# Optimization experiments

Measured on AMD Instinct MI355X. Metric: run time of the kernel, lower is better.

## Reference

```python
import jax, jax.numpy as jnp
import numpy as np

B, T, C = 4, 2048, 1024
NH = 16
HD = C // NH  # 64


def setup_inputs() -> dict:
    key = jax.random.key(0)
    k1, k2, k3 = jax.random.split(key, 3)
    x = jax.random.normal(k1, (B, T, C), dtype=jnp.float32)
    # causal mask buffer, 1 = keep, 0 = mask out
    mask = jnp.tril(jnp.ones((T, T), dtype=jnp.int32))[None, None, :, :]
    # learned params (Linear with bias=False): torch stores weight as [out, in],
    # y = x @ W.T ; we store transposed for direct matmul
    w_qkv = jax.random.normal(k2, (C, 3 * C), dtype=jnp.float32) / np.sqrt(C)
    w_proj = jax.random.normal(k3, (C, C), dtype=jnp.float32) / np.sqrt(C)
    return {"x": x, "mask": mask, "w_qkv": w_qkv, "w_proj": w_proj}


def reference(x, mask, w_qkv, w_proj):
    b, t, c = x.shape
    qkv = x @ w_qkv  # [b, t, 3c]
    q, k, v = jnp.split(qkv, 3, axis=-1)
    # [b, nh, t, hd]
    q = q.reshape(b, t, NH, HD).transpose(0, 2, 1, 3)
    k = k.reshape(b, t, NH, HD).transpose(0, 2, 1, 3)
    v = v.reshape(b, t, NH, HD).transpose(0, 2, 1, 3)
    att = jnp.einsum("bhqd,bhkd->bhqk", q, k) * (1.0 / np.sqrt(HD))
    att = jnp.where(mask == 0, -jnp.inf, att)
    att = jax.nn.softmax(att, axis=-1)
    y = jnp.einsum("bhqk,bhkd->bhqd", att, v)
    y = y.transpose(0, 2, 1, 3).reshape(b, t, c)
    return y @ w_proj
```

## Files before the change

kernel.cpp:

```cpp
#include <hip/hip_runtime.h>
#include <hip/hip_bf16.h>

typedef _Float16 f16;
typedef __attribute__((ext_vector_type(4))) _Float16 f16x4;
typedef __attribute__((ext_vector_type(8))) _Float16 f16x8;
typedef __attribute__((ext_vector_type(4))) float f32x4;

#define MFMA16(a, b, c) __builtin_amdgcn_mfma_f32_16x16x16f16((a), (b), (c), 0, 0, 0)
#define MFMA32(a, b, c) __builtin_amdgcn_mfma_f32_16x16x32_f16((a), (b), (c), 0, 0, 0)
#define EXP2(x) __builtin_amdgcn_exp2f(x)
#define GLOAD_LDS16(g, l)                                                        \
  __builtin_amdgcn_global_load_lds((const __attribute__((address_space(1))) void*)(g), \
                                   (__attribute__((address_space(3))) void*)(l), 16, 0, 0)
typedef const __attribute__((address_space(3))) char* lds_cp;
#define TR16(dst, addr, imm) \
  asm volatile("ds_read_b64_tr_b16 %0, %1 offset:" imm : "=v"(dst) : "v"(addr))

__device__ __forceinline__ float max3f(float a, float b, float c) {
  return fmaxf(fmaxf(a, b), c);
}

__global__ __launch_bounds__(256) void prep_kernel(
    const float* __restrict__ x, f16* __restrict__ x16,
    const float* __restrict__ wq, f16* __restrict__ wqT,
    const float* __restrict__ wp, f16* __restrict__ wpT) {
  const int blk = blockIdx.x;
  const int tid = threadIdx.x;
  if (blk < 8192) {
    int i = blk * 256 + tid;
    const float4 v = reinterpret_cast<const float4*>(x)[i];
    f16x4 h;
    h[0] = (f16)v.x; h[1] = (f16)v.y; h[2] = (f16)v.z; h[3] = (f16)v.w;
    reinterpret_cast<f16x4*>(x16)[i] = h;
    return;
  }
  const float* src;
  f16* dst;
  int R, Cc, bx, by;
  if (blk < 11264) {
    int j = blk - 8192;
    bx = j % 96; by = j / 96;
    src = wq; dst = wqT; R = 1024; Cc = 3072;
  } else {
    int j = blk - 11264;
    bx = j & 31; by = j >> 5;
    src = wp; dst = wpT; R = 1024; Cc = 1024;
  }
  __shared__ float t[32][33];
  int tx0 = bx * 32, ty0 = by * 32;
  int c = tid & 31;
  int r0 = tid >> 5;
#pragma unroll
  for (int i = 0; i < 4; i++) {
    int r = r0 + 8 * i;
    t[r][c] = src[(size_t)(ty0 + r) * Cc + tx0 + c];
  }
  __syncthreads();
#pragma unroll
  for (int i = 0; i < 4; i++) {
    int a = r0 + 8 * i;
    dst[(size_t)(tx0 + a) * R + ty0 + c] = (f16)t[c][a];
  }
}

template <bool OUT_F32>
__global__ __launch_bounds__(512, 2) void gemm_deep_kernel(
    const f16* __restrict__ A, const f16* __restrict__ Bt, void* __restrict__ Cout,
    int M, int N, int K) {
  __shared__ __align__(16) char smem[147456];
  const int tid = threadIdx.x;
  const int lane = tid & 63, wid = tid >> 6;
  const int wm = wid >> 2, wn = wid & 3;
  const int lo = lane & 15, hi = lane >> 4;

  const int ntn = N >> 7;
  const int nwg = (M >> 8) * ntn;
  const int wg = (blockIdx.x & 7) * (nwg >> 3) + (blockIdx.x >> 3);
  const int tm0 = (wg / ntn) << 8;
  const int tn0 = (wg % ntn) << 7;

  const int prow = tid >> 3;
  const int u8 = (tid & 7) ^ (prow & 7);
  const f16* asrc[4];
  const f16* bsrc[2];
#pragma unroll
  for (int c = 0; c < 4; c++) asrc[c] = A + (size_t)(tm0 + c * 64 + prow) * K + u8 * 8;
#pragma unroll
  for (int c = 0; c < 2; c++) bsrc[c] = Bt + (size_t)(tn0 + c * 64 + prow) * K + u8 * 8;

  const int swz = lo & 7;
  const int s0 = (hi ^ swz) << 4, s1 = ((4 + hi) ^ swz) << 4;
  const int abase0 = wm * 16384 + lo * 128 + s0;
  const int abase1 = wm * 16384 + lo * 128 + s1;
  int boff0[2], boff1[2];
#pragma unroll
  for (int ni = 0; ni < 2; ni++) {
    int g = 2 * wn + ni;
    int base = 32768 + (g >> 2) * 8192 + ((g & 3) * 16 + lo) * 128;
    boff0[ni] = base + s0;
    boff1[ni] = base + s1;
  }

  f32x4 acc[8][2] = {};

  auto stage = [&](int kt, char* buf) {
    const int ke = kt << 6;
#pragma unroll
    for (int c = 0; c < 4; c++)
      GLOAD_LDS16(asrc[c] + ke, buf + c * 8192 + tid * 16);
#pragma unroll
    for (int c = 0; c < 2; c++)
      GLOAD_LDS16(bsrc[c] + ke, buf + 32768 + c * 8192 + tid * 16);
  };

  const int NT = K >> 6;
  stage(0, smem);
  stage(1, smem + 49152);

  int bufi = 0;
  for (int t = 0; t < NT; t++) {
    char* db = smem + bufi * 49152;
    if (t + 1 < NT) {
      asm volatile("s_waitcnt vmcnt(6)" ::: "memory");
    } else {
      asm volatile("s_waitcnt vmcnt(0)" ::: "memory");
    }
    __builtin_amdgcn_s_barrier();
    if (t + 2 < NT) {
      int nb = bufi + 2;
      if (nb >= 3) nb -= 3;
      stage(t + 2, smem + nb * 49152);
    }
    __builtin_amdgcn_sched_barrier(0);

    f16x8 a[8][2], b[2][2];
#pragma unroll
    for (int mi = 0; mi < 8; mi++) {
      int off = (mi >> 2) * 8192 + (mi & 3) * 2048;
      a[mi][0] = *(const f16x8*)(db + abase0 + off);
      a[mi][1] = *(const f16x8*)(db + abase1 + off);
    }
#pragma unroll
    for (int ni = 0; ni < 2; ni++) {
      b[ni][0] = *(const f16x8*)(db + boff0[ni]);
      b[ni][1] = *(const f16x8*)(db + boff1[ni]);
    }
    __builtin_amdgcn_s_setprio(1);
#pragma unroll
    for (int mi = 0; mi < 8; mi++)
#pragma unroll
      for (int ni = 0; ni < 2; ni++) {
        acc[mi][ni] = MFMA32(a[mi][0], b[ni][0], acc[mi][ni]);
        acc[mi][ni] = MFMA32(a[mi][1], b[ni][1], acc[mi][ni]);
      }
    __builtin_amdgcn_s_setprio(0);

    bufi = (bufi == 2) ? 0 : bufi + 1;
  }

#pragma unroll
  for (int mi = 0; mi < 8; mi++)
#pragma unroll
    for (int ni = 0; ni < 2; ni++)
#pragma unroll
      for (int r = 0; r < 4; r++) {
        int row = tm0 + wm * 128 + mi * 16 + 4 * hi + r;
        int col = tn0 + wn * 32 + ni * 16 + lo;
        float v = acc[mi][ni][r];
        if (OUT_F32)
          ((float*)Cout)[(size_t)row * N + col] = v;
        else
          ((f16*)Cout)[(size_t)row * N + col] = (f16)v;
      }
}

__global__ __launch_bounds__(256, 4) void attn_kernel(
    const f16* __restrict__ qkv, f16* __restrict__ y) {
  constexpr int T = 2048, NHD = 3072, LDO = 72;
  const int bh = blockIdx.x;
  const int b = bh >> 4, h = bh & 15;
  const int pr = blockIdx.y;
  const int tid = threadIdx.x;
  const int lane = tid & 63, w = tid >> 6;
  const int lo = lane & 15, hi = lane >> 4;

  const size_t base = (size_t)b * T * NHD + (size_t)h * 64;
  const f16* Qp = qkv + base;
  const f16* Kp = qkv + base + 1024;
  const f16* Vp = qkv + base + 2048;

  __shared__ __align__(16) char smem[32768];
  f16 (*Ol)[LDO] = (f16(*)[LDO])smem;

  const int tile[2] = {pr, 31 - pr};
  const int qb[2] = {tile[0] * 64 + w * 16, tile[1] * 64 + w * 16};

  const float scf = 0.125f * 1.44269504089f;
  f16x8 qf[2][2];
#pragma unroll
  for (int s = 0; s < 2; s++) {
    const f16* qrow = Qp + (size_t)(qb[s] + lo) * NHD;
#pragma unroll
    for (int ks = 0; ks < 2; ks++) {
      f16x8 v = *(const f16x8*)&qrow[ks * 32 + 8 * hi];
#pragma unroll
      for (int j = 0; j < 8; j++) v[j] = (f16)((float)v[j] * scf);
      qf[s][ks] = v;
    }
  }

  f32x4 oacc[2][4] = {};
  f32x4 lacc[2] = {};
  float mreg[2] = {-1e30f, -1e30f};
  const f16x4 ones4 = {(f16)1.f, (f16)1.f, (f16)1.f, (f16)1.f};

  const int kr = tid >> 3;
  const int kslot = (tid & 7) ^ (kr & 7);
  const int tp = tid & 127;
  const int vkey = 4 * (tp >> 3) + ((tp >> 1) & 3);
  const int vcol = (tid >> 7) * 16 + (tid & 1) * 8;

  const int kfo0 = lo * 64 + ((hi ^ (lo & 7)) * 8);
  const int kfo1 = lo * 64 + (((4 + hi) ^ (lo & 7)) * 8);

  auto stage = [&](int kv, int c) {
    char* kb = smem + c * 8192;
    char* vb = smem + 16384 + c * 8192;
    GLOAD_LDS16(&Kp[(size_t)(kv + kr) * NHD + kslot * 8], kb + tid * 16);
    GLOAD_LDS16(&Kp[(size_t)(kv + kr + 32) * NHD + kslot * 8], kb + 4096 + tid * 16);
    GLOAD_LDS16(&Vp[(size_t)(kv + vkey) * NHD + vcol], vb + tid * 16);
    GLOAD_LDS16(&Vp[(size_t)(kv + vkey) * NHD + vcol + 32], vb + 4096 + tid * 16);
  };

  const int nt = 32 - pr;
  stage(0, 0);
  asm volatile("s_waitcnt vmcnt(0)" ::: "memory");
  __builtin_amdgcn_s_barrier();

  for (int t = 0; t < nt; t++) {
    const int cur = t & 1;
    const int kv0 = t * 64;
    if (t + 1 < nt) stage(kv0 + 64, cur ^ 1);

    const f16* Kl = (const f16*)(smem + cur * 8192);
    const bool act0 = kv0 <= qb[0] + 15;

    f16x8 kf[2][4];
#pragma unroll
    for (int ct = 0; ct < 4; ct++) {
      kf[0][ct] = *(const f16x8*)&Kl[ct * 1024 + kfo0];
      kf[1][ct] = *(const f16x8*)&Kl[ct * 1024 + kfo1];
    }

    f16x4 pb[2][4];
#pragma unroll
    for (int s = 0; s < 2; s++) {
      if (s == 0 && !act0) continue;
      f32x4 s_[4] = {};
      __builtin_amdgcn_s_setprio(1);
#pragma unroll
      for (int ks = 0; ks < 2; ks++)
#pragma unroll
        for (int ct = 0; ct < 4; ct++)
          s_[ct] = MFMA32(kf[ks][ct], qf[s][ks], s_[ct]);
      __builtin_amdgcn_s_setprio(0);

      if (kv0 + 63 > qb[s]) {
        const int q = qb[s] + lo;
#pragma unroll
        for (int ct = 0; ct < 4; ct++)
#pragma unroll
          for (int r = 0; r < 4; r++)
            if (kv0 + ct * 16 + 4 * hi + r > q) s_[ct][r] = -3.0e38f;
      }
      float t0 = max3f(s_[0][0], s_[0][1], s_[0][2]);
      float t1 = max3f(s_[0][3], s_[1][0], s_[1][1]);
      float t2 = max3f(s_[1][2], s_[1][3], s_[2][0]);
      float t3 = max3f(s_[2][1], s_[2][2], s_[2][3]);
      float t4 = max3f(s_[3][0], s_[3][1], s_[3][2]);
      float mt = fmaxf(max3f(t0, t1, t2), max3f(t3, t4, s_[3][3]));
      mt = fmaxf(mt, __shfl_xor(mt, 16));
      mt = fmaxf(mt, __shfl_xor(mt, 32));
      float mn = mreg[s];
      if (!__all(mt <= mn + 8.f)) {
        mn = fmaxf(mn, mt);
        const float al = EXP2(mreg[s] - mn);
        mreg[s] = mn;
#pragma unroll
        for (int r = 0; r < 4; r++) lacc[s][r] *= al;
#pragma unroll
        for (int ct = 0; ct < 4; ct++)
#pragma unroll
          for (int r = 0; r < 4; r++) oacc[s][ct][r] *= al;
      }
#pragma unroll
      for (int ct = 0; ct < 4; ct++)
#pragma unroll
        for (int r = 0; r < 4; r++)
          pb[s][ct][r] = (f16)EXP2(s_[ct][r] - mn);
      __builtin_amdgcn_s_setprio(1);
#pragma unroll
      for (int kk = 0; kk < 4; kk++)
        lacc[s] = MFMA16(ones4, pb[s][kk], lacc[s]);
      __builtin_amdgcn_s_setprio(0);
    }

    lds_cp vtrb = (lds_cp)(smem + 16384 + cur * 8192) + lane * 8;
#pragma unroll
    for (int ct = 0; ct < 4; ct++) {
      lds_cp bct = vtrb + ct * 2048;
      f16x4 v0, v1, v2, v3;
      TR16(v0, bct, "0");
      TR16(v1, bct, "512");
      TR16(v2, bct, "1024");
      TR16(v3, bct, "1536");
      asm volatile("s_waitcnt lgkmcnt(0)" ::: "memory");
      __builtin_amdgcn_sched_barrier(0);
      __builtin_amdgcn_s_setprio(1);
      if (act0) {
        oacc[0][ct] = MFMA16(v0, pb[0][0], oacc[0][ct]);
        oacc[0][ct] = MFMA16(v1, pb[0][1], oacc[0][ct]);
        oacc[0][ct] = MFMA16(v2, pb[0][2], oacc[0][ct]);
        oacc[0][ct] = MFMA16(v3, pb[0][3], oacc[0][ct]);
      }
      oacc[1][ct] = MFMA16(v0, pb[1][0], oacc[1][ct]);
      oacc[1][ct] = MFMA16(v1, pb[1][1], oacc[1][ct]);
      oacc[1][ct] = MFMA16(v2, pb[1][2], oacc[1][ct]);
      oacc[1][ct] = MFMA16(v3, pb[1][3], oacc[1][ct]);
      __builtin_amdgcn_s_setprio(0);
    }

    asm volatile("s_waitcnt vmcnt(0)" ::: "memory");
    __builtin_amdgcn_s_barrier();
  }

#pragma unroll
  for (int s = 0; s < 2; s++) {
    __syncthreads();
    const float inv = 1.f / lacc[s][0];
#pragma unroll
    for (int ct = 0; ct < 4; ct++) {
      f16x4 o4;
#pragma unroll
      for (int r = 0; r < 4; r++) o4[r] = (f16)(oacc[s][ct][r] * inv);
      *(f16x4*)&Ol[w * 16 + lo][ct * 16 + 4 * hi] = o4;
    }
    __syncthreads();
#pragma unroll
    for (int i = 0; i < 2; i++) {
      int idx = tid + 256 * i;
      int qq = idx >> 3, ch = idx & 7;
      *(f16x8*)&y[((size_t)b * T + tile[s] * 64 + qq) * 1024 + (size_t)h * 64 + ch * 8] =
          *(const f16x8*)&Ol[qq][ch * 8];
    }
  }
}

extern "C" void kernel_launch(void* const* d_in, const int* in_sizes, int n_in,
                              void* d_out, int out_size, void* d_ws, size_t ws_size,
                              hipStream_t stream) {
  const float* x = (const float*)d_in[0];
  const float* w_qkv = (const float*)d_in[2];
  const float* w_proj = (const float*)d_in[3];

  constexpr int B = 4, T = 2048, C = 1024, NH = 16;
  constexpr int M = B * T;
  constexpr int N1 = 3 * C;

  char* ws = (char*)d_ws;
  f16* x16 = (f16*)ws;    ws += (size_t)M * C * 2;
  f16* wqkvT = (f16*)ws;  ws += (size_t)N1 * C * 2;
  f16* wprojT = (f16*)ws; ws += (size_t)C * C * 2;
  f16* qkvb = (f16*)ws;   ws += (size_t)M * N1 * 2;
  f16* y16 = (f16*)ws;

  prep_kernel<<<12288, 256, 0, stream>>>(x, x16, w_qkv, wqkvT, w_proj, wprojT);
  gemm_deep_kernel<false><<<(M / 256) * (N1 / 128), 512, 0, stream>>>(x16, wqkvT, qkvb, M, N1, C);
  attn_kernel<<<dim3(B * NH, 16), 256, 0, stream>>>(qkvb, y16);
  gemm_deep_kernel<true><<<(M / 256) * (C / 128), 512, 0, stream>>>(y16, wprojT, (float*)d_out, M, C, C);
}
```

Measured before the change: 172.6 us.

## Reorder attention inner loop to issue both QK MFMAs first and interleave softmax with PV

Restructures the per-tile loop so both sub-tiles' QK^T MFMAs are issued back to back. Each sub-tile's softmax is then immediately followed by its own PV accumulation instead of doing all softmax before all PV. The fp32-to-f16 conversion of probabilities now uses packed round-toward-zero conversion. The aim is to overlap MFMA latency with exp/max ALU work and cut conversion instructions, at the cost of holding more score registers live and slightly different rounding. V fragments are now read from LDS twice per tile, once per sub-tile.

```diff
diff --git a/kernel.cpp b/kernel.cpp
--- a/kernel.cpp
+++ b/kernel.cpp
@@ -2,6 +2,7 @@
 #include <hip/hip_bf16.h>
 
 typedef _Float16 f16;
+typedef __attribute__((ext_vector_type(2))) __fp16 fp16x2;
 typedef __attribute__((ext_vector_type(4))) _Float16 f16x4;
 typedef __attribute__((ext_vector_type(8))) _Float16 f16x8;
 typedef __attribute__((ext_vector_type(4))) float f32x4;
@@ -232,80 +233,52 @@
     GLOAD_LDS16(&Vp[(size_t)(kv + vkey) * NHD + vcol + 32], vb + 4096 + tid * 16);
   };
 
-  const int nt = 32 - pr;
-  stage(0, 0);
-  asm volatile("s_waitcnt vmcnt(0)" ::: "memory");
-  __builtin_amdgcn_s_barrier();
-
-  for (int t = 0; t < nt; t++) {
-    const int cur = t & 1;
-    const int kv0 = t * 64;
-    if (t + 1 < nt) stage(kv0 + 64, cur ^ 1);
-
-    const f16* Kl = (const f16*)(smem + cur * 8192);
-    const bool act0 = kv0 <= qb[0] + 15;
-
-    f16x8 kf[2][4];
+  auto softmax_fin = [&](f32x4* sv, int si, f16x4* pbv, int kv0) {
+    if (kv0 + 63 > qb[si]) {
+      const int q = qb[si] + lo;
+#pragma unroll
+      for (int ct = 0; ct < 4; ct++)
+#pragma unroll
+        for (int r = 0; r < 4; r++)
+          if (kv0 + ct * 16 + 4 * hi + r > q) sv[ct][r] = -3.0e38f;
+    }
+    float t0 = max3f(sv[0][0], sv[0][1], sv[0][2]);
+    float t1 = max3f(sv[0][3], sv[1][0], sv[1][1]);
+    float t2 = max3f(sv[1][2], sv[1][3], sv[2][0]);
+    float t3 = max3f(sv[2][1], sv[2][2], sv[2][3]);
+    float t4 = max3f(sv[3][0], sv[3][1], sv[3][2]);
+    float mt = fmaxf(max3f(t0, t1, t2), max3f(t3, t4, sv[3][3]));
+    mt = fmaxf(mt, __shfl_xor(mt, 16));
+    mt = fmaxf(mt, __shfl_xor(mt, 32));
+    float mn = mreg[si];
+    if (!__all(mt <= mn + 8.f)) {
+      mn = fmaxf(mn, mt);
+      const float al = EXP2(mreg[si] - mn);
+      mreg[si] = mn;
+#pragma unroll
+      for (int r = 0; r < 4; r++) lacc[si][r] *= al;
+#pragma unroll
+      for (int ct = 0; ct < 4; ct++)
+#pragma unroll
+        for (int r = 0; r < 4; r++) oacc[si][ct][r] *= al;
+    }
 #pragma unroll
     for (int ct = 0; ct < 4; ct++) {
-      kf[0][ct] = *(const f16x8*)&Kl[ct * 1024 + kfo0];
-      kf[1][ct] = *(const f16x8*)&Kl[ct * 1024 + kfo1];
-    }
-
-    f16x4 pb[2][4];
-#pragma unroll
-    for (int s = 0; s < 2; s++) {
-      if (s == 0 && !act0) continue;
-      f32x4 s_[4] = {};
-      __builtin_amdgcn_s_setprio(1);
-#pragma unroll
-      for (int ks = 0; ks < 2; ks++)
-#pragma unroll
-        for (int ct = 0; ct < 4; ct++)
-          s_[ct] = MFMA32(kf[ks][ct], qf[s][ks], s_[ct]);
-      __builtin_amdgcn_s_setprio(0);
-
-      if (kv0 + 63 > qb[s]) {
-        const int q = qb[s] + lo;
-#pragma unroll
-        for (int ct = 0; ct < 4; ct++)
-#pragma unroll
-          for (int r = 0; r < 4; r++)
-            if (kv0 + ct * 16 + 4 * hi + r > q) s_[ct][r] = -3.0e38f;
-      }
-      float t0 = max3f(s_[0][0], s_[0][1], s_[0][2]);
-      float t1 = max3f(s_[0][3], s_[1][0], s_[1][1]);
-      float t2 = max3f(s_[1][2], s_[1][3], s_[2][0]);
-      float t3 = max3f(s_[2][1], s_[2][2], s_[2][3]);
-      float t4 = max3f(s_[3][0], s_[3][1], s_[3][2]);
-      float mt = fmaxf(max3f(t0, t1, t2), max3f(t3, t4, s_[3][3]));
-      mt = fmaxf(mt, __shfl_xor(mt, 16));
-      mt = fmaxf(mt, __shfl_xor(mt, 32));
-      float mn = mreg[s];
-      if (!__all(mt <= mn + 8.f)) {
-        mn = fmaxf(mn, mt);
-        const float al = EXP2(mreg[s] - mn);
-        mreg[s] = mn;
-#pragma unroll
-        for (int r = 0; r < 4; r++) lacc[s][r] *= al;
-#pragma unroll
-        for (int ct = 0; ct < 4; ct++)
-#pragma unroll
-          for (int r = 0; r < 4; r++) oacc[s][ct][r] *= al;
-      }
-#pragma unroll
-      for (int ct = 0; ct < 4; ct++)
-#pragma unroll
-        for (int r = 0; r < 4; r++)
-          pb[s][ct][r] = (f16)EXP2(s_[ct][r] - mn);
-      __builtin_amdgcn_s_setprio(1);
-#pragma unroll
-      for (int kk = 0; kk < 4; kk++)
-        lacc[s] = MFMA16(ones4, pb[s][kk], lacc[s]);
-      __builtin_amdgcn_s_setprio(0);
-    }
-
-    lds_cp vtrb = (lds_cp)(smem + 16384 + cur * 8192) + lane * 8;
+      float p0 = EXP2(sv[ct][0] - mn), p1 = EXP2(sv[ct][1] - mn);
+      float p2 = EXP2(sv[ct][2] - mn), p3 = EXP2(sv[ct][3] - mn);
+      union { f16x4 v; fp16x2 h[2]; } u;
+      u.h[0] = __builtin_amdgcn_cvt_pkrtz(p0, p1);
+      u.h[1] = __builtin_amdgcn_cvt_pkrtz(p2, p3);
+      pbv[ct] = u.v;
+    }
+    __builtin_amdgcn_s_setprio(1);
+#pragma unroll
+    for (int kk = 0; kk < 4; kk++)
+      lacc[si] = MFMA16(ones4, pbv[kk], lacc[si]);
+    __builtin_amdgcn_s_setprio(0);
+  };
+
+  auto pv_sub = [&](int si, f16x4* pbv, lds_cp vtrb) {
 #pragma unroll
     for (int ct = 0; ct < 4; ct++) {
       lds_cp bct = vtrb + ct * 2048;
@@ -317,17 +290,67 @@
       asm volatile("s_waitcnt lgkmcnt(0)" ::: "memory");
       __builtin_amdgcn_sched_barrier(0);
       __builtin_amdgcn_s_setprio(1);
-      if (act0) {
-        oacc[0][ct] = MFMA16(v0, pb[0][0], oacc[0][ct]);
-        oacc[0][ct] = MFMA16(v1, pb[0][1], oacc[0][ct]);
-        oacc[0][ct] = MFMA16(v2, pb[0][2], oacc[0][ct]);
-        oacc[0][ct] = MFMA16(v3, pb[0][3], oacc[0][ct]);
-      }
-      oacc[1][ct] = MFMA16(v0, pb[1][0], oacc[1][ct]);
-      oacc[1][ct] = MFMA16(v1, pb[1][1], oacc[1][ct]);
-      oacc[1][ct] = MFMA16(v2, pb[1][2], oacc[1][ct]);
-      oacc[1][ct] = MFMA16(v3, pb[1][3], oacc[1][ct]);
+      oacc[si][ct] = MFMA16(v0, pbv[0], oacc[si][ct]);
+      oacc[si][ct] = MFMA16(v1, pbv[1], oacc[si][ct]);
+      oacc[si][ct] = MFMA16(v2, pbv[2], oacc[si][ct]);
+      oacc[si][ct] = MFMA16(v3, pbv[3], oacc[si][ct]);
       __builtin_amdgcn_s_setprio(0);
+    }
+  };
+
+  const int nt = 32 - pr;
+  stage(0, 0);
+  asm volatile("s_waitcnt vmcnt(0)" ::: "memory");
+  __builtin_amdgcn_s_barrier();
+
+  for (int t = 0; t < nt; t++) {
+    const int cur = t & 1;
+    const int kv0 = t * 64;
+    if (t + 1 < nt) stage(kv0 + 64, cur ^ 1);
+
+    const f16* Kl = (const f16*)(smem + cur * 8192);
+    const bool act0 = kv0 <= qb[0] + 15;
+
+    f16x8 kf[2][4];
+#pragma unroll
+    for (int ct = 0; ct < 4; ct++) {
+      kf[0][ct] = *(const f16x8*)&Kl[ct * 1024 + kfo0];
+      kf[1][ct] = *(const f16x8*)&Kl[ct * 1024 + kfo1];
+    }
+
+    lds_cp vtrb = (lds_cp)(smem + 16384 + cur * 8192) + lane * 8;
+    f16x4 pb0[4], pb1[4];
+
+    if (act0) {
+      f32x4 s0_[4] = {}, s1_[4] = {};
+      __builtin_amdgcn_s_setprio(1);
+#pragma unroll
+      for (int ks = 0; ks < 2; ks++)
+#pragma unroll
+        for (int ct = 0; ct < 4; ct++)
+          s0_[ct] = MFMA32(kf[ks][ct], qf[0][ks], s0_[ct]);
+#pragma unroll
+      for (int ks = 0; ks < 2; ks++)
+#pragma unroll
+        for (int ct = 0; ct < 4; ct++)
+          s1_[ct] = MFMA32(kf[ks][ct], qf[1][ks], s1_[ct]);
+      __builtin_amdgcn_s_setprio(0);
+
+      softmax_fin(s0_, 0, pb0, kv0);
+      pv_sub(0, pb0, vtrb);
+      softmax_fin(s1_, 1, pb1, kv0);
+      pv_sub(1, pb1, vtrb);
+    } else {
+      f32x4 s1_[4] = {};
+      __builtin_amdgcn_s_setprio(1);
+#pragma unroll
+      for (int ks = 0; ks < 2; ks++)
+#pragma unroll
+        for (int ct = 0; ct < 4; ct++)
+          s1_[ct] = MFMA32(kf[ks][ct], qf[1][ks], s1_[ct]);
+      __builtin_amdgcn_s_setprio(0);
+      softmax_fin(s1_, 1, pb1, kv0);
+      pv_sub(1, pb1, vtrb);
     }
 
     asm volatile("s_waitcnt vmcnt(0)" ::: "memory");
```

Result: no change. 173.8 us (+0.7%).

## Split attention tile pair across 8 waves instead of 4 per block

Applied to the files above, without the earlier changes.

The attention block grows to 512 threads, and each wave owns 16 query rows from one of the two paired tiles instead of 32 rows spread across both. This halves per-wave register state and serialized work, and the cooperative K/V staging now takes one load each per thread. V transposed reads are hoisted ahead of the softmax so they overlap it, and the P conversion uses packed round-toward-zero conversions. Waves on the short tile sit idle once they pass the causal diagonal, and the final write reuses the shared buffer for all 128 rows.

```diff
diff --git a/kernel.cpp b/kernel.cpp
--- a/kernel.cpp
+++ b/kernel.cpp
@@ -2,6 +2,7 @@
 #include <hip/hip_bf16.h>
 
 typedef _Float16 f16;
+typedef __attribute__((ext_vector_type(2))) __fp16 fp16x2;
 typedef __attribute__((ext_vector_type(4))) _Float16 f16x4;
 typedef __attribute__((ext_vector_type(8))) _Float16 f16x8;
 typedef __attribute__((ext_vector_type(4))) float f32x4;
@@ -174,7 +175,7 @@
       }
 }
 
-__global__ __launch_bounds__(256, 4) void attn_kernel(
+__global__ __launch_bounds__(512, 2) void attn_kernel(
     const f16* __restrict__ qkv, f16* __restrict__ y) {
   constexpr int T = 2048, NHD = 3072, LDO = 72;
   const int bh = blockIdx.x;
@@ -192,32 +193,30 @@
   __shared__ __align__(16) char smem[32768];
   f16 (*Ol)[LDO] = (f16(*)[LDO])smem;
 
-  const int tile[2] = {pr, 31 - pr};
-  const int qb[2] = {tile[0] * 64 + w * 16, tile[1] * 64 + w * 16};
+  const int mytile = (w < 4) ? pr : (31 - pr);
+  const int qb = mytile * 64 + (w & 3) * 16;
 
   const float scf = 0.125f * 1.44269504089f;
-  f16x8 qf[2][2];
-#pragma unroll
-  for (int s = 0; s < 2; s++) {
-    const f16* qrow = Qp + (size_t)(qb[s] + lo) * NHD;
+  f16x8 qf[2];
+  {
+    const f16* qrow = Qp + (size_t)(qb + lo) * NHD;
 #pragma unroll
     for (int ks = 0; ks < 2; ks++) {
       f16x8 v = *(const f16x8*)&qrow[ks * 32 + 8 * hi];
 #pragma unroll
       for (int j = 0; j < 8; j++) v[j] = (f16)((float)v[j] * scf);
-      qf[s][ks] = v;
-    }
-  }
-
-  f32x4 oacc[2][4] = {};
-  f32x4 lacc[2] = {};
-  float mreg[2] = {-1e30f, -1e30f};
+      qf[ks] = v;
+    }
+  }
+
+  f32x4 oacc[4] = {};
+  f32x4 lacc = {};
+  float mreg = -1e30f;
   const f16x4 ones4 = {(f16)1.f, (f16)1.f, (f16)1.f, (f16)1.f};
 
   const int kr = tid >> 3;
   const int kslot = (tid & 7) ^ (kr & 7);
-  const int tp = tid & 127;
-  const int vkey = 4 * (tp >> 3) + ((tp >> 1) & 3);
+  const int vkey = 4 * ((tid & 127) >> 3) + ((tid >> 1) & 3);
   const int vcol = (tid >> 7) * 16 + (tid & 1) * 8;
 
   const int kfo0 = lo * 64 + ((hi ^ (lo & 7)) * 8);
@@ -227,9 +226,7 @@
     char* kb = smem + c * 8192;
     char* vb = smem + 16384 + c * 8192;
     GLOAD_LDS16(&Kp[(size_t)(kv + kr) * NHD + kslot * 8], kb + tid * 16);
-    GLOAD_LDS16(&Kp[(size_t)(kv + kr + 32) * NHD + kslot * 8], kb + 4096 + tid * 16);
     GLOAD_LDS16(&Vp[(size_t)(kv + vkey) * NHD + vcol], vb + tid * 16);
-    GLOAD_LDS16(&Vp[(size_t)(kv + vkey) * NHD + vcol + 32], vb + 4096 + tid * 16);
   };
 
   const int nt = 32 - pr;
@@ -242,31 +239,35 @@
     const int kv0 = t * 64;
     if (t + 1 < nt) stage(kv0 + 64, cur ^ 1);
 
-    const f16* Kl = (const f16*)(smem + cur * 8192);
-    const bool act0 = kv0 <= qb[0] + 15;
-
-    f16x8 kf[2][4];
-#pragma unroll
-    for (int ct = 0; ct < 4; ct++) {
-      kf[0][ct] = *(const f16x8*)&Kl[ct * 1024 + kfo0];
-      kf[1][ct] = *(const f16x8*)&Kl[ct * 1024 + kfo1];
-    }
-
-    f16x4 pb[2][4];
-#pragma unroll
-    for (int s = 0; s < 2; s++) {
-      if (s == 0 && !act0) continue;
+    if (kv0 <= qb + 15) {
+      const f16* Kl = (const f16*)(smem + cur * 8192);
+      f16x8 kf0[4], kf1[4];
+#pragma unroll
+      for (int ct = 0; ct < 4; ct++) {
+        kf0[ct] = *(const f16x8*)&Kl[ct * 1024 + kfo0];
+        kf1[ct] = *(const f16x8*)&Kl[ct * 1024 + kfo1];
+      }
       f32x4 s_[4] = {};
       __builtin_amdgcn_s_setprio(1);
 #pragma unroll
-      for (int ks = 0; ks < 2; ks++)
-#pragma unroll
-        for (int ct = 0; ct < 4; ct++)
-          s_[ct] = MFMA32(kf[ks][ct], qf[s][ks], s_[ct]);
+      for (int ct = 0; ct < 4; ct++) s_[ct] = MFMA32(kf0[ct], qf[0], s_[ct]);
+#pragma unroll
+      for (int ct = 0; ct < 4; ct++) s_[ct] = MFMA32(kf1[ct], qf[1], s_[ct]);
       __builtin_amdgcn_s_setprio(0);
 
-      if (kv0 + 63 > qb[s]) {
-        const int q = qb[s] + lo;
+      lds_cp vtrb = (lds_cp)(smem + 16384 + cur * 8192) + lane * 8;
+      f16x4 v[4][4];
+#pragma unroll
+      for (int ct = 0; ct < 4; ct++) {
+        lds_cp bct = vtrb + ct * 2048;
+        TR16(v[ct][0], bct, "0");
+        TR16(v[ct][1], bct, "512");
+        TR16(v[ct][2], bct, "1024");
+        TR16(v[ct][3], bct, "1536");
+      }
+
+      if (kv0 + 63 > qb) {
+        const int q = qb + lo;
 #pragma unroll
         for (int ct = 0; ct < 4; ct++)
 #pragma unroll
@@ -281,52 +282,43 @@
       float mt = fmaxf(max3f(t0, t1, t2), max3f(t3, t4, s_[3][3]));
       mt = fmaxf(mt, __shfl_xor(mt, 16));
       mt = fmaxf(mt, __shfl_xor(mt, 32));
-      float mn = mreg[s];
+      float mn = mreg;
       if (!__all(mt <= mn + 8.f)) {
         mn = fmaxf(mn, mt);
-        const float al = EXP2(mreg[s] - mn);
-        mreg[s] = mn;
-#pragma unroll
-        for (int r = 0; r < 4; r++) lacc[s][r] *= al;
+        const float al = EXP2(mreg - mn);
+        mreg = mn;
+#pragma unroll
+        for (int r = 0; r < 4; r++) lacc[r] *= al;
 #pragma unroll
         for (int ct = 0; ct < 4; ct++)
 #pragma unroll
-          for (int r = 0; r < 4; r++) oacc[s][ct][r] *= al;
-      }
-#pragma unroll
-      for (int ct = 0; ct < 4; ct++)
-#pragma unroll
-        for (int r = 0; r < 4; r++)
-          pb[s][ct][r] = (f16)EXP2(s_[ct][r] - mn);
+          for (int r = 0; r < 4; r++) oacc[ct][r] *= al;
+      }
+      f16x4 pb[4];
+#pragma unroll
+      for (int ct = 0; ct < 4; ct++) {
+        float p0 = EXP2(s_[ct][0] - mn), p1 = EXP2(s_[ct][1] - mn);
+        float p2 = EXP2(s_[ct][2] - mn), p3 = EXP2(s_[ct][3] - mn);
+        union { f16x4 vv; fp16x2 hh[2]; } u;
+        u.hh[0] = __builtin_amdgcn_cvt_pkrtz(p0, p1);
+        u.hh[1] = __builtin_amdgcn_cvt_pkrtz(p2, p3);
+        pb[ct] = u.vv;
+      }
       __builtin_amdgcn_s_setprio(1);
 #pragma unroll
-      for (int kk = 0; kk < 4; kk++)
-        lacc[s] = MFMA16(ones4, pb[s][kk], lacc[s]);
+      for (int kk = 0; kk < 4; kk++) lacc = MFMA16(ones4, pb[kk], lacc);
       __builtin_amdgcn_s_setprio(0);
-    }
-
-    lds_cp vtrb = (lds_cp)(smem + 16384 + cur * 8192) + lane * 8;
-#pragma unroll
-    for (int ct = 0; ct < 4; ct++) {
-      lds_cp bct = vtrb + ct * 2048;
-      f16x4 v0, v1, v2, v3;
-      TR16(v0, bct, "0");
-      TR16(v1, bct, "512");
-      TR16(v2, bct, "1024");
-      TR16(v3, bct, "1536");
+
       asm volatile("s_waitcnt lgkmcnt(0)" ::: "memory");
       __builtin_amdgcn_sched_barrier(0);
       __builtin_amdgcn_s_setprio(1);
-      if (act0) {
-        oacc[0][ct] = MFMA16(v0, pb[0][0], oacc[0][ct]);
-        oacc[0][ct] = MFMA16(v1, pb[0][1], oacc[0][ct]);
-        oacc[0][ct] = MFMA16(v2, pb[0][2], oacc[0][ct]);
-        oacc[0][ct] = MFMA16(v3, pb[0][3], oacc[0][ct]);
-      }
-      oacc[1][ct] = MFMA16(v0, pb[1][0], oacc[1][ct]);
-      oacc[1][ct] = MFMA16(v1, pb[1][1], oacc[1][ct]);
-      oacc[1][ct] = MFMA16(v2, pb[1][2], oacc[1][ct]);
-      oacc[1][ct] = MFMA16(v3, pb[1][3], oacc[1][ct]);
+#pragma unroll
+      for (int ct = 0; ct < 4; ct++) {
+        oacc[ct] = MFMA16(v[ct][0], pb[0], oacc[ct]);
+        oacc[ct] = MFMA16(v[ct][1], pb[1], oacc[ct]);
+        oacc[ct] = MFMA16(v[ct][2], pb[2], oacc[ct]);
+        oacc[ct] = MFMA16(v[ct][3], pb[3], oacc[ct]);
+      }
       __builtin_amdgcn_s_setprio(0);
     }
 
@@ -334,25 +326,22 @@
     __builtin_amdgcn_s_barrier();
   }
 
-#pragma unroll
-  for (int s = 0; s < 2; s++) {
-    __syncthreads();
-    const float inv = 1.f / lacc[s][0];
-#pragma unroll
-    for (int ct = 0; ct < 4; ct++) {
-      f16x4 o4;
-#pragma unroll
-      for (int r = 0; r < 4; r++) o4[r] = (f16)(oacc[s][ct][r] * inv);
-      *(f16x4*)&Ol[w * 16 + lo][ct * 16 + 4 * hi] = o4;
-    }
-    __syncthreads();
-#pragma unroll
-    for (int i = 0; i < 2; i++) {
-      int idx = tid + 256 * i;
-      int qq = idx >> 3, ch = idx & 7;
-      *(f16x8*)&y[((size_t)b * T + tile[s] * 64 + qq) * 1024 + (size_t)h * 64 + ch * 8] =
-          *(const f16x8*)&Ol[qq][ch * 8];
-    }
+  const float inv = 1.f / lacc[0];
+#pragma unroll
+  for (int ct = 0; ct < 4; ct++) {
+    f16x4 o4;
+#pragma unroll
+    for (int r = 0; r < 4; r++) o4[r] = (f16)(oacc[ct][r] * inv);
+    *(f16x4*)&Ol[w * 16 + lo][ct * 16 + 4 * hi] = o4;
+  }
+  __syncthreads();
+#pragma unroll
+  for (int i = 0; i < 2; i++) {
+    int idx = tid + 512 * i;
+    int qq = idx >> 3, ch = idx & 7;
+    int row = ((qq < 64) ? pr : (31 - pr)) * 64 + (qq & 63);
+    *(f16x8*)&y[((size_t)b * T + row) * 1024 + (size_t)h * 64 + ch * 8] =
+        *(const f16x8*)&Ol[qq][ch * 8];
   }
 }
 
@@ -376,6 +365,6 @@
 
   prep_kernel<<<12288, 256, 0, stream>>>(x, x16, w_qkv, wqkvT, w_proj, wprojT);
   gemm_deep_kernel<false><<<(M / 256) * (N1 / 128), 512, 0, stream>>>(x16, wqkvT, qkvb, M, N1, C);
-  attn_kernel<<<dim3(B * NH, 16), 256, 0, stream>>>(qkvb, y16);
+  attn_kernel<<<dim3(B * NH, 16), 512, 0, stream>>>(qkvb, y16);
   gemm_deep_kernel<true><<<(M / 256) * (C / 128), 512, 0, stream>>>(y16, wprojT, (float*)d_out, M, C, C);
 }
```

New measurement: 172.2 us. About the same (-0.2%).
